# Kernel optimization log

Measured on AMD Instinct MI355X. Metric: run time of the kernel, lower is better.

The kernel has to match this reference:

```python
import jax, jax.numpy as jnp
import numpy as np

B, N = 4, 8192
D = 128
DEPTH = 4
LEAF = 32
HEADS = 4
HD = D // HEADS
SLOTS = 24
RANKS = [20, 32, 52, 82]                      # rank at encoder step j (fine -> coarse)
EXP = [RANKS[j] * (2 ** j) for j in range(DEPTH)]  # HODLR head output dims


def _rope_tables(seq_len, dim):
    inv_freq = 1.0 / (10000.0 ** (jnp.arange(0, dim, 2, dtype=jnp.float32) / dim))
    t = jnp.arange(seq_len, dtype=jnp.float32)
    freqs = t[:, None] * inv_freq[None, :]
    emb = jnp.concatenate([freqs, freqs], axis=-1)   # [S, dim]
    return jnp.cos(emb), jnp.sin(emb)


def _rotate_half(x):
    x1, x2 = jnp.split(x, 2, axis=-1)
    return jnp.concatenate([-x2, x1], axis=-1)


def _layernorm(x, g, b, eps=1e-5):
    mu = jnp.mean(x, -1, keepdims=True)
    var = jnp.mean((x - mu) ** 2, -1, keepdims=True)
    return (x - mu) * jax.lax.rsqrt(var + eps) * g + b


def _block_attn(h, qkv_w, qkv_b, pw, pb, cos, sin):
    Bc, Nc, C = h.shape
    nb = Nc // LEAF
    xb = h.reshape(Bc * nb, LEAF, C)
    qkv = (xb @ qkv_w + qkv_b).reshape(Bc * nb, LEAF, 3, HEADS, HD)
    qkv = qkv.transpose(2, 0, 3, 1, 4)               # [3, BN, H, L, hd]
    q, k, v = qkv[0], qkv[1], qkv[2]
    q = q * cos + _rotate_half(q) * sin              # full-dim RoPE (rope_dim == head_dim)
    k = k * cos + _rotate_half(k) * sin
    attn = jax.nn.softmax(jnp.einsum('bhqd,bhkd->bhqk', q, k) * (HD ** -0.5), axis=-1)
    o = jnp.einsum('bhqk,bhkd->bhqd', attn, v).transpose(0, 2, 1, 3).reshape(Bc * nb, LEAF, C)
    return (o @ pw + pb).reshape(Bc, Nc, C)


def _forward(x, cen_w, cen_b, nbr_w, nbr_b, inp_w, inp_b,
             leafp_w, leafp_b, leafh_w, leafh_b, log_scale_leaf,
             ln1_g, ln1_b, qkv_w, qkv_b, attnp_w, attnp_b,
             ln2_g, ln2_b, mlp1_w, mlp1_b, mlp2_w, mlp2_b, ds_w, ds_b,
             hu_w0, hu_b0, hv_w0, hv_b0, hu_w1, hu_b1, hv_w1, hv_b1,
             hu_w2, hu_b2, hv_w2, hv_b2, hu_w3, hu_b3, hv_w3, hv_b3):
    Bx, Nx, _ = x.shape
    # --- SymmetricNeighborEmbed (24 neighbor slots, vectorized) ---
    pos_i = x[..., 0:3]
    diag_i = x[..., 3:4]
    h_center = jnp.concatenate([pos_i, diag_i], -1) @ cen_w + cen_b          # [B,N,D]
    nb_feat = x[..., 4:4 + 5 * SLOTS].reshape(Bx, Nx, SLOTS, 5)
    rel = nb_feat[..., 0:1]
    pos_j = nb_feat[..., 1:4]
    w_ij = nb_feat[..., 4:5]
    active = (w_ij != 0.0).astype(x.dtype)
    feat = jnp.concatenate([rel * active, (pos_j - pos_i[:, :, None, :]) * active, w_ij], -1)
    e = (feat @ nbr_w + nbr_b) * active                                       # [B,N,24,D]
    h = h_center + jnp.sum(e, axis=2)
    h = h @ inp_w + inp_b
    # --- leaf dense diagonal blocks ---
    nl = Nx // LEAF
    hl = h.reshape(Bx, nl, LEAF, D) @ leafp_w + leafp_b                       # [B,nl,32,32]
    u_leaf = hl @ leafh_w + leafh_b
    dense = jnp.einsum('blik,bljk->blij', u_leaf, u_leaf) * jnp.exp(log_scale_leaf)
    diag_a = x[..., 3]                                                        # scale_A defaults to 1.0
    mask = jnp.abs(diag_a) > 1e-6
    new_diag = jnp.where(mask, 1.0 / jnp.where(mask, diag_a, 1.0), 1.0).reshape(Bx, nl, LEAF)
    dense = dense + new_diag[..., :, None] * jnp.eye(LEAF, dtype=x.dtype)
    # --- down-only encoder: transformer block -> HODLR head -> 2:1 downsample ---
    cos, sin = _rope_tables(LEAF, HD)
    hu = [(hu_w0, hu_b0), (hu_w1, hu_b1), (hu_w2, hu_b2), (hu_w3, hu_b3)]
    hv = [(hv_w0, hv_b0), (hv_w1, hv_b1), (hv_w2, hv_b2), (hv_w3, hv_b3)]
    us, vs = [], []
    for j in range(DEPTH):
        a = _block_attn(_layernorm(h, ln1_g[j], ln1_b[j]),
                        qkv_w[j], qkv_b[j], attnp_w[j], attnp_b[j], cos, sin)
        h = h + a
        m = _layernorm(h, ln2_g[j], ln2_b[j])
        m = jax.nn.gelu(m @ mlp1_w[j] + mlp1_b[j], approximate=False) @ mlp2_w[j] + mlp2_b[j]
        h = h + m
        us.append((h @ hu[j][0] + hu[j][1]).reshape(Bx, Nx, RANKS[j]))
        vs.append((h @ hv[j][0] + hv[j][1]).reshape(Bx, Nx, RANKS[j]))
        Bh, n, c = h.shape
        h = h.reshape(Bh, n // 2, 2 * c) @ ds_w[j] + ds_b[j]
    # single flat output: dense leaf blocks + all U/V HODLR factors
    return jnp.concatenate([dense.reshape(Bx, -1),
                            jnp.concatenate(us, -1).reshape(Bx, -1),
                            jnp.concatenate(vs, -1).reshape(Bx, -1)], -1)


def setup_inputs():
    key = jax.random.key(0)
    ks = iter(jax.random.split(key, 64))
    def rn(shape, s=0.05):
        return jax.random.normal(next(ks), shape, jnp.float32) * s
    z = lambda *s: jnp.zeros(s, jnp.float32)
    o = lambda *s: jnp.ones(s, jnp.float32)
    inp = {
        'x': jax.random.normal(next(ks), (B, N, 4 + 5 * SLOTS), jnp.float32),
        'cen_w': rn((4, D)), 'cen_b': z(D),
        'nbr_w': rn((5, D)), 'nbr_b': z(D),
        'inp_w': rn((D, D)), 'inp_b': z(D),
        'leafp_w': rn((D, LEAF)), 'leafp_b': z(LEAF),
        'leafh_w': rn((LEAF, LEAF), 0.01), 'leafh_b': z(LEAF),
        'log_scale_leaf': jnp.full((1,), np.log(0.01), jnp.float32),
        'ln1_g': o(DEPTH, D), 'ln1_b': z(DEPTH, D),
        'qkv_w': rn((DEPTH, D, 3 * D)), 'qkv_b': z(DEPTH, 3 * D),
        'attnp_w': rn((DEPTH, D, D)), 'attnp_b': z(DEPTH, D),
        'ln2_g': o(DEPTH, D), 'ln2_b': z(DEPTH, D),
        'mlp1_w': rn((DEPTH, D, 4 * D)), 'mlp1_b': z(DEPTH, 4 * D),
        'mlp2_w': rn((DEPTH, 4 * D, D)), 'mlp2_b': z(DEPTH, D),
        'ds_w': rn((DEPTH, 2 * D, D)), 'ds_b': z(DEPTH, D),
    }
    for j in range(DEPTH):
        inp['hu_w%d' % j] = rn((D, EXP[j]), 0.01)
        inp['hu_b%d' % j] = z(EXP[j])
        inp['hv_w%d' % j] = rn((D, EXP[j]), 0.01)
        inp['hv_b%d' % j] = z(EXP[j])
    return inp


def reference(x, cen_w, cen_b, nbr_w, nbr_b, inp_w, inp_b,
              leafp_w, leafp_b, leafh_w, leafh_b, log_scale_leaf,
              ln1_g, ln1_b, qkv_w, qkv_b, attnp_w, attnp_b,
              ln2_g, ln2_b, mlp1_w, mlp1_b, mlp2_w, mlp2_b, ds_w, ds_b,
              hu_w0, hu_b0, hv_w0, hv_b0, hu_w1, hu_b1, hv_w1, hv_b1,
              hu_w2, hu_b2, hv_w2, hv_b2, hu_w3, hu_b3, hv_w3, hv_b3):
    return _forward(x, cen_w, cen_b, nbr_w, nbr_b, inp_w, inp_b,
                    leafp_w, leafp_b, leafh_w, leafh_b, log_scale_leaf,
                    ln1_g, ln1_b, qkv_w, qkv_b, attnp_w, attnp_b,
                    ln2_g, ln2_b, mlp1_w, mlp1_b, mlp2_w, mlp2_b, ds_w, ds_b,
                    hu_w0, hu_b0, hv_w0, hv_b0, hu_w1, hu_b1, hv_w1, hv_b1,
                    hu_w2, hu_b2, hv_w2, hv_b2, hu_w3, hu_b3, hv_w3, hv_b3)
```

## Files before the change

kernel.cpp:

```cpp
#include <hip/hip_runtime.h>
#include <math.h>

#define DEV __device__ __forceinline__

constexpr int XFv = 124;
constexpr size_t OPB   = 3309568;
constexpr size_t UBASE = 262144;
constexpr size_t VBASE = 1785856;
constexpr int UVWID = 186;

using bfrag  = __attribute__((ext_vector_type(8))) short;
using f32x4v = __attribute__((ext_vector_type(4))) float;

DEV float* at4p(float* base, int t, int c0, int W) {
  return base + t * W + ((c0 + 4 * t) & (W - 1));
}
DEV float& at1r(float* base, int t, int c, int W) {
  return base[t * W + (((c & ~3) + 4 * t) & (W - 1)) + (c & 3)];
}
DEV float4 ld4g(const float* p) { return *(const float4*)p; }
DEV void fma4(float4& a, float s, const float4& w) {
  a.x += s * w.x; a.y += s * w.y; a.z += s * w.z; a.w += s * w.w;
}
DEV float gelu_fast(float x) {
  float x2 = x * x;
  float z = x * (1.5957691216057308f + 0.0713551f * x2);
  float e = __expf(z);
  float r = 1.0f - __frcp_rn(e + 1.0f);
  return x * r;
}
DEV ushort f2bf(float x) {
  unsigned u = __float_as_uint(x);
  unsigned r = (u + 0x7fffu + ((u >> 16) & 1u)) >> 16;
  return (ushort)r;
}
DEV void stb128(ushort* b, int row, int col, float v) {
  b[row * 128 + (((col & ~7) + 8 * row) & 127) + (col & 7)] = f2bf(v);
}

__global__ __launch_bounds__(256) void wprep_all_kernel(
    const float* __restrict__ src0, ushort* __restrict__ dst0, int K, int N) {
  size_t off = (size_t)blockIdx.z * K * N;
  const float* src = src0 + off;
  ushort* dst = dst0 + off;
  __shared__ float S[64][65];
  int tid = threadIdx.x;
  int k0 = blockIdx.x * 64, n0 = blockIdx.y * 64;
  for (int i = tid; i < 64 * 64; i += 256) {
    int kk = i >> 6, nn = i & 63;
    S[kk][nn] = src[(size_t)(k0 + kk) * N + n0 + nn];
  }
  __syncthreads();
  int n = tid >> 2, kq = tid & 3;
  unsigned pk[8];
#pragma unroll
  for (int i = 0; i < 8; i++) {
    int k = kq * 16 + 2 * i;
    pk[i] = (unsigned)f2bf(S[k][n]) | ((unsigned)f2bf(S[k + 1][n]) << 16);
  }
  unsigned* dp = (unsigned*)&dst[(size_t)(n0 + n) * K + k0 + kq * 16];
#pragma unroll
  for (int i = 0; i < 8; i++) dp[i] = pk[i];
}

struct UVDesc {
  const float* src[8];
  ushort* dst[8];
  int expj[8];
  int npad[8];
};
__global__ __launch_bounds__(256) void uvprep_all_kernel(UVDesc d) {
  int mi = blockIdx.y;
  int i = blockIdx.x * 256 + threadIdx.x;
  int expj = d.expj[mi];
  if (i >= d.npad[mi] * 128) return;
  int n = i >> 7, k = i & 127;
  d.dst[mi][(size_t)n * 128 + k] =
      (n < expj) ? f2bf(d.src[mi][(size_t)k * expj + n]) : (ushort)0;
}

__global__ __launch_bounds__(128) void weff_prep_kernel(
    const float* __restrict__ cw, const float* __restrict__ cb,
    const float* __restrict__ nw, const float* __restrict__ nb,
    const float* __restrict__ iw, const float* __restrict__ ib,
    float* __restrict__ weff, float* __restrict__ ropetab) {
  __shared__ float S[11 * 128];
  int tid = threadIdx.x;
  for (int i = tid; i < 512; i += 128) S[i] = cw[i];
  for (int i = tid; i < 640; i += 128) S[512 + i] = nw[i];
  S[1152 + tid] = nb[tid];
  S[1280 + tid] = cb[tid];
  __syncthreads();
  float acc[11];
#pragma unroll
  for (int r = 0; r < 10; r++) acc[r] = 0.f;
  acc[10] = ib[tid];
  for (int k = 0; k < 128; k++) {
    float w = iw[k * 128 + tid];
#pragma unroll
    for (int r = 0; r < 11; r++) acc[r] += S[r * 128 + k] * w;
  }
#pragma unroll
  for (int r = 0; r < 11; r++) weff[r * 128 + tid] = acc[r];
  for (int idx = tid; idx < 512; idx += 128) {
    int pos = idx >> 4, d = idx & 15;
    float ang = (float)pos * expf(-0.57564627324851148f * (float)d);
    ropetab[idx] = cosf(ang);
    ropetab[512 + idx] = sinf(ang);
  }
}

__global__ __launch_bounds__(256) void node_embed2_kernel(
    const float* __restrict__ x, const float* __restrict__ weff,
    float* __restrict__ h) {
  __shared__ float XR[64 * XFv];
  __shared__ float RF[64][11];
  __shared__ __align__(16) float WE[11 * 128];
  int tid = threadIdx.x;
  int node0 = blockIdx.x * 64;
  for (int i = tid; i < 64 * XFv; i += 256)
    XR[i] = x[(size_t)node0 * XFv + i];
  for (int i = tid; i < 11 * 128; i += 256) WE[i] = weff[i];
  __syncthreads();
  {
    int nn = tid >> 2, sl = tid & 3;
    const float* xr = XR + nn * XFv;
    float p0 = xr[0], p1 = xr[1], p2 = xr[2];
    float g[6] = {0.f, 0.f, 0.f, 0.f, 0.f, 0.f};
#pragma unroll
    for (int s = 0; s < 6; s++) {
      const float* f = xr + 4 + 5 * (sl * 6 + s);
      float w = f[4];
      if (w != 0.0f) {
        g[0] += f[0]; g[1] += f[1] - p0; g[2] += f[2] - p1;
        g[3] += f[3] - p2; g[4] += w; g[5] += 1.0f;
      }
    }
#pragma unroll
    for (int i = 0; i < 6; i++) {
      g[i] += __shfl_xor(g[i], 1);
      g[i] += __shfl_xor(g[i], 2);
    }
    if (sl == 0) {
      RF[nn][0] = p0; RF[nn][1] = p1; RF[nn][2] = p2; RF[nn][3] = xr[3];
#pragma unroll
      for (int i = 0; i < 6; i++) RF[nn][4 + i] = g[i];
    }
  }
  __syncthreads();
  {
    int w = tid >> 6, lane = tid & 63;
    int c4 = lane & 31, hi = lane >> 5;
    const float4* WE4 = (const float4*)WE;
#pragma unroll
    for (int rr = 0; rr < 8; rr++) {
      int node = w * 16 + rr * 2 + hi;
      float4 acc = WE4[10 * 32 + c4];
#pragma unroll
      for (int f = 0; f < 10; f++)
        fma4(acc, RF[node][f], WE4[f * 32 + c4]);
      *(float4*)&h[(size_t)(node0 + node) * 128 + c4 * 4] = acc;
    }
  }
}

__global__ __launch_bounds__(256) void leaf_dense_kernel(
    const float* __restrict__ h, const float* __restrict__ x,
    const float* __restrict__ lpw, const float* __restrict__ lpb,
    const float* __restrict__ lhw, const float* __restrict__ lhb,
    const float* __restrict__ lsc, float* __restrict__ out) {
  __shared__ __align__(16) float HS[32 * 128];
  __shared__ __align__(16) float HL[32 * 32];
  __shared__ __align__(16) float UL[32 * 32];
  int tid = threadIdx.x;
  int leaf = blockIdx.x;
  size_t base = (size_t)leaf * (32 * 128);
  for (int i = tid; i < 32 * 128; i += 256) {
    int t = i >> 7, c = i & 127;
    at1r(HS, t, c, 128) = h[base + i];
  }
  __syncthreads();
  int t = tid & 31, cg = tid >> 5;
  {
    float4 acc = ld4g(&lpb[4 * cg]);
    for (int k4 = 0; k4 < 128; k4 += 4) {
      float4 xv = *(const float4*)at4p(HS, t, k4, 128);
      float xa[4] = {xv.x, xv.y, xv.z, xv.w};
#pragma unroll
      for (int kk = 0; kk < 4; kk++)
        fma4(acc, xa[kk], ld4g(&lpw[(k4 + kk) * 32 + 4 * cg]));
    }
    *(float4*)at4p(HL, t, 4 * cg, 32) = acc;
  }
  __syncthreads();
  {
    float4 acc = ld4g(&lhb[4 * cg]);
    for (int k4 = 0; k4 < 32; k4 += 4) {
      float4 xv = *(const float4*)at4p(HL, t, k4, 32);
      float xa[4] = {xv.x, xv.y, xv.z, xv.w};
#pragma unroll
      for (int kk = 0; kk < 4; kk++)
        fma4(acc, xa[kk], ld4g(&lhw[(k4 + kk) * 32 + 4 * cg]));
    }
    *(float4*)at4p(UL, t, 4 * cg, 32) = acc;
  }
  __syncthreads();
  {
    float scale = expf(lsc[0]);
    float acc[4] = {0.f, 0.f, 0.f, 0.f};
    for (int k4 = 0; k4 < 32; k4 += 4) {
      float4 xv = *(const float4*)at4p(UL, t, k4, 32);
      float xa[4] = {xv.x, xv.y, xv.z, xv.w};
#pragma unroll
      for (int kk = 0; kk < 4; kk++) {
        int k = k4 + kk;
#pragma unroll
        for (int i2 = 0; i2 < 4; i2++)
          acc[i2] += xa[kk] * at1r(UL, 4 * cg + i2, k, 32);
      }
    }
    int b = leaf >> 8, l = leaf & 255;
#pragma unroll
    for (int i2 = 0; i2 < 4; i2++) {
      int c = 4 * cg + i2;
      float v = acc[i2] * scale;
      if (c == t) {
        float dg = x[(size_t)(leaf * 32 + t) * XFv + 3];
        v += (fabsf(dg) > 1e-6f) ? (1.0f / dg) : 1.0f;
      }
      out[(size_t)b * OPB + (size_t)l * 1024 + t * 32 + c] = v;
    }
  }
}

__global__ __launch_bounds__(256) void attn_mfma_kernel(
    float* __restrict__ h,
    const float* __restrict__ lng, const float* __restrict__ lnb,
    const ushort* __restrict__ wqkvt, const float* __restrict__ bqkv,
    const ushort* __restrict__ wpt, const float* __restrict__ pb,
    const float* __restrict__ rt) {
  __shared__ __align__(16) ushort XN[64 * 128];
  __shared__ __align__(16) ushort QB[64 * 128];
  __shared__ __align__(16) ushort KB[64 * 128];
  __shared__ __align__(16) ushort VT[128 * 64];
  int tid = threadIdx.x;
  size_t base = (size_t)blockIdx.x * (64 * 128);

  {
    int m = tid >> 2, p = tid & 3;
    const float* row = h + base + m * 128 + p * 32;
    float v[32];
    float s = 0.f;
#pragma unroll
    for (int i = 0; i < 32; i += 4) {
      float4 t4 = ld4g(row + i);
      v[i] = t4.x; v[i + 1] = t4.y; v[i + 2] = t4.z; v[i + 3] = t4.w;
      s += t4.x + t4.y + t4.z + t4.w;
    }
    s += __shfl_xor(s, 1); s += __shfl_xor(s, 2);
    float mu = s * (1.0f / 128.0f);
    float s2 = 0.f;
#pragma unroll
    for (int i = 0; i < 32; i++) { float d = v[i] - mu; s2 += d * d; }
    s2 += __shfl_xor(s2, 1); s2 += __shfl_xor(s2, 2);
    float rs = rsqrtf(s2 * (1.0f / 128.0f) + 1e-5f);
    unsigned* XW = (unsigned*)XN;
#pragma unroll
    for (int i = 0; i < 32; i += 2) {
      int c = p * 32 + i;
      float x0 = (v[i] - mu) * rs * lng[c] + lnb[c];
      float x1 = (v[i + 1] - mu) * rs * lng[c + 1] + lnb[c + 1];
      int kp = c >> 1;
      XW[m * 64 + ((kp + 4 * m) & 63)] =
          (unsigned)f2bf(x0) | ((unsigned)f2bf(x1) << 16);
    }
  }
  __syncthreads();

  int w = tid >> 6, l = tid & 63, lm = l & 15, q = l >> 4;

  {
    f32x4v acc[4][6];
#pragma unroll
    for (int mt = 0; mt < 4; mt++)
#pragma unroll
      for (int nt = 0; nt < 6; nt++) acc[mt][nt] = (f32x4v){0.f, 0.f, 0.f, 0.f};
    for (int ks = 0; ks < 4; ks++) {
      bfrag a[4];
#pragma unroll
      for (int mt = 0; mt < 4; mt++) {
        int mm = mt * 16 + lm;
        a[mt] = *(const bfrag*)&XN[mm * 128 + ((ks * 32 + q * 8 + 8 * mm) & 127)];
      }
#pragma unroll
      for (int nt = 0; nt < 6; nt++) {
        int n = w * 96 + nt * 16 + lm;
        bfrag b = *(const bfrag*)&wqkvt[(size_t)n * 128 + ks * 32 + q * 8];
#pragma unroll
        for (int mt = 0; mt < 4; mt++)
          acc[mt][nt] = __builtin_amdgcn_mfma_f32_16x16x32_bf16(
              a[mt], b, acc[mt][nt], 0, 0, 0);
      }
    }
    float csA[4] = {}, snA[4] = {}, csB[4] = {}, snB[4] = {};
    if (w < 3) {
#pragma unroll
      for (int r = 0; r < 4; r++) {
        int pa = q * 4 + r;
        csA[r] = rt[pa * 16 + lm];        snA[r] = rt[512 + pa * 16 + lm];
        csB[r] = rt[(pa + 16) * 16 + lm]; snB[r] = rt[512 + (pa + 16) * 16 + lm];
      }
    }
#pragma unroll
    for (int p2 = 0; p2 < 3; p2++) {
      int g = w * 6 + 2 * p2;
      int ne = g * 16 + lm;
      if (g < 16) {
        float be = bqkv[ne], bo = bqkv[ne + 16];
        ushort* dst = (g < 8) ? QB : KB;
        int de = (g < 8) ? ne : ne - 128;
#pragma unroll
        for (int mt = 0; mt < 4; mt++)
#pragma unroll
          for (int r = 0; r < 4; r++) {
            int mm = mt * 16 + q * 4 + r;
            float cs = (mt & 1) ? csB[r] : csA[r];
            float sn = (mt & 1) ? snB[r] : snA[r];
            float e = acc[mt][2 * p2][r] + be;
            float o = acc[mt][2 * p2 + 1][r] + bo;
            stb128(dst, mm, de, e * cs - o * sn);
            stb128(dst, mm, de + 16, o * cs + e * sn);
          }
      } else {
#pragma unroll
        for (int h2 = 0; h2 < 2; h2++) {
          int nt = 2 * p2 + h2;
          int nv = (g + h2) * 16 + lm;
          int dv = nv - 256;
          float bv = bqkv[nv];
#pragma unroll
          for (int mt = 0; mt < 4; mt++) {
            int t0 = mt * 16 + q * 4;
            short4 pk;
            pk.x = (short)f2bf(acc[mt][nt][0] + bv);
            pk.y = (short)f2bf(acc[mt][nt][1] + bv);
            pk.z = (short)f2bf(acc[mt][nt][2] + bv);
            pk.w = (short)f2bf(acc[mt][nt][3] + bv);
            *(short4*)&VT[dv * 64 + (((t0 & ~7) + 8 * dv) & 63) + (t0 & 7)] = pk;
          }
        }
      }
    }
  }
  __syncthreads();

  ushort* SP = XN;
  {
#pragma unroll
    for (int ci = 0; ci < 2; ci++) {
      int combo = w + 4 * ci;
      int head = combo >> 1, leaf = combo & 1;
      f32x4v sc[2][2];
#pragma unroll
      for (int a2 = 0; a2 < 2; a2++)
#pragma unroll
        for (int b2 = 0; b2 < 2; b2++) sc[a2][b2] = (f32x4v){0.f, 0.f, 0.f, 0.f};
      bfrag qa[2], kb[2];
#pragma unroll
      for (int mt2 = 0; mt2 < 2; mt2++) {
        int row = leaf * 32 + mt2 * 16 + lm;
        qa[mt2] = *(const bfrag*)&QB[row * 128 + ((head * 32 + q * 8 + 8 * row) & 127)];
      }
#pragma unroll
      for (int nt2 = 0; nt2 < 2; nt2++) {
        int kt = leaf * 32 + nt2 * 16 + lm;
        kb[nt2] = *(const bfrag*)&KB[kt * 128 + ((head * 32 + q * 8 + 8 * kt) & 127)];
      }
#pragma unroll
      for (int mt2 = 0; mt2 < 2; mt2++)
#pragma unroll
        for (int nt2 = 0; nt2 < 2; nt2++)
          sc[mt2][nt2] = __builtin_amdgcn_mfma_f32_16x16x32_bf16(
              qa[mt2], kb[nt2], sc[mt2][nt2], 0, 0, 0);
      const float scl = 0.17677669529663688f;
#pragma unroll
      for (int mt2 = 0; mt2 < 2; mt2++)
#pragma unroll
        for (int nt2 = 0; nt2 < 2; nt2++)
#pragma unroll
          for (int r = 0; r < 4; r++) {
            int qt = leaf * 32 + mt2 * 16 + q * 4 + r;
            int kc = nt2 * 16 + lm;
            SP[head * 2048 + qt * 32 + (((kc & ~7) + 8 * qt) & 31) + (kc & 7)] =
                f2bf(sc[mt2][nt2][r] * scl);
          }
    }
  }
  __syncthreads();

  {
    int head = tid >> 6, qt = tid & 63;
    ushort* rowp = SP + head * 2048 + qt * 32;
    float v[32];
#pragma unroll
    for (int pc = 0; pc < 4; pc++) {
      uint4 ch = *(const uint4*)&rowp[pc * 8];
      unsigned uu[4] = {ch.x, ch.y, ch.z, ch.w};
#pragma unroll
      for (int i2 = 0; i2 < 4; i2++) {
        v[pc * 8 + 2 * i2]     = __uint_as_float(uu[i2] << 16);
        v[pc * 8 + 2 * i2 + 1] = __uint_as_float(uu[i2] & 0xffff0000u);
      }
    }
    float mx = -1e30f;
#pragma unroll
    for (int i = 0; i < 32; i++) mx = fmaxf(mx, v[i]);
    float s = 0.f;
#pragma unroll
    for (int i = 0; i < 32; i++) { v[i] = __expf(v[i] - mx); s += v[i]; }
    float inv = 1.0f / s;
#pragma unroll
    for (int pc = 0; pc < 4; pc++) {
      uint4 ch;
      unsigned uu[4];
#pragma unroll
      for (int i2 = 0; i2 < 4; i2++)
        uu[i2] = (unsigned)f2bf(v[pc * 8 + 2 * i2] * inv) |
                 ((unsigned)f2bf(v[pc * 8 + 2 * i2 + 1] * inv) << 16);
      ch.x = uu[0]; ch.y = uu[1]; ch.z = uu[2]; ch.w = uu[3];
      *(uint4*)&rowp[pc * 8] = ch;
    }
  }
  __syncthreads();

  ushort* OB = QB;
  {
#pragma unroll
    for (int ci = 0; ci < 2; ci++) {
      int combo = w + 4 * ci;
      int head = combo >> 1, leaf = combo & 1;
      f32x4v ov[2][2];
#pragma unroll
      for (int a2 = 0; a2 < 2; a2++)
#pragma unroll
        for (int b2 = 0; b2 < 2; b2++) ov[a2][b2] = (f32x4v){0.f, 0.f, 0.f, 0.f};
      bfrag pa[2], vb[2];
#pragma unroll
      for (int mt2 = 0; mt2 < 2; mt2++) {
        int qt = leaf * 32 + mt2 * 16 + lm;
        pa[mt2] = *(const bfrag*)&SP[head * 2048 + qt * 32 + ((q * 8 + 8 * qt) & 31)];
      }
#pragma unroll
      for (int nt2 = 0; nt2 < 2; nt2++) {
        int gdim = head * 32 + nt2 * 16 + lm;
        int t0 = leaf * 32 + q * 8;
        vb[nt2] = *(const bfrag*)&VT[gdim * 64 + ((t0 + 8 * gdim) & 63)];
      }
#pragma unroll
      for (int mt2 = 0; mt2 < 2; mt2++)
#pragma unroll
        for (int nt2 = 0; nt2 < 2; nt2++)
          ov[mt2][nt2] = __builtin_amdgcn_mfma_f32_16x16x32_bf16(
              pa[mt2], vb[nt2], ov[mt2][nt2], 0, 0, 0);
#pragma unroll
      for (int mt2 = 0; mt2 < 2; mt2++)
#pragma unroll
        for (int nt2 = 0; nt2 < 2; nt2++)
#pragma unroll
          for (int r = 0; r < 4; r++) {
            int qt = leaf * 32 + mt2 * 16 + q * 4 + r;
            int gdim = head * 32 + nt2 * 16 + lm;
            stb128(OB, qt, gdim, ov[mt2][nt2][r]);
          }
    }
  }
  __syncthreads();

  {
    f32x4v po[4][2];
#pragma unroll
    for (int mt = 0; mt < 4; mt++)
#pragma unroll
      for (int nt = 0; nt < 2; nt++) po[mt][nt] = (f32x4v){0.f, 0.f, 0.f, 0.f};
    for (int ks = 0; ks < 4; ks++) {
      bfrag a[4];
#pragma unroll
      for (int mt = 0; mt < 4; mt++) {
        int mm = mt * 16 + lm;
        a[mt] = *(const bfrag*)&OB[mm * 128 + ((ks * 32 + q * 8 + 8 * mm) & 127)];
      }
#pragma unroll
      for (int nt = 0; nt < 2; nt++) {
        int n = w * 32 + nt * 16 + lm;
        bfrag b = *(const bfrag*)&wpt[(size_t)n * 128 + ks * 32 + q * 8];
#pragma unroll
        for (int mt = 0; mt < 4; mt++)
          po[mt][nt] = __builtin_amdgcn_mfma_f32_16x16x32_bf16(
              a[mt], b, po[mt][nt], 0, 0, 0);
      }
    }
#pragma unroll
    for (int nt = 0; nt < 2; nt++) {
      int n = w * 32 + nt * 16 + lm;
      float bv = pb[n];
#pragma unroll
      for (int mt = 0; mt < 4; mt++)
#pragma unroll
        for (int r = 0; r < 4; r++) {
          int mm = mt * 16 + q * 4 + r;
          float* gp = h + base + (size_t)mm * 128 + n;
          *gp = *gp + po[mt][nt][r] + bv;
        }
    }
  }
}

__global__ __launch_bounds__(256) void mlp_mfma_kernel(
    float* __restrict__ h,
    const float* __restrict__ lng, const float* __restrict__ lnb,
    const ushort* __restrict__ w1t, const float* __restrict__ b1,
    const ushort* __restrict__ w2t, const float* __restrict__ b2) {
  __shared__ __align__(16) ushort XN[64 * 128];
  __shared__ __align__(16) ushort HC[64 * 128];
  int tid = threadIdx.x;
  size_t base = (size_t)blockIdx.x * (64 * 128);

  {
    int m = tid >> 2, p = tid & 3;
    const float* row = h + base + m * 128 + p * 32;
    float v[32];
    float s = 0.f;
#pragma unroll
    for (int i = 0; i < 32; i += 4) {
      float4 t4 = ld4g(row + i);
      v[i] = t4.x; v[i + 1] = t4.y; v[i + 2] = t4.z; v[i + 3] = t4.w;
      s += t4.x + t4.y + t4.z + t4.w;
    }
    s += __shfl_xor(s, 1); s += __shfl_xor(s, 2);
    float mu = s * (1.0f / 128.0f);
    float s2 = 0.f;
#pragma unroll
    for (int i = 0; i < 32; i++) { float d = v[i] - mu; s2 += d * d; }
    s2 += __shfl_xor(s2, 1); s2 += __shfl_xor(s2, 2);
    float rs = rsqrtf(s2 * (1.0f / 128.0f) + 1e-5f);
    unsigned* XW = (unsigned*)XN;
#pragma unroll
    for (int i = 0; i < 32; i += 2) {
      int c = p * 32 + i;
      float x0 = (v[i] - mu) * rs * lng[c] + lnb[c];
      float x1 = (v[i + 1] - mu) * rs * lng[c + 1] + lnb[c + 1];
      int kp = c >> 1;
      XW[m * 64 + ((kp + 4 * m) & 63)] =
          (unsigned)f2bf(x0) | ((unsigned)f2bf(x1) << 16);
    }
  }
  __syncthreads();

  int w = tid >> 6, l = tid & 63, lm = l & 15, q = l >> 4;

  f32x4v acc2[4][2];
#pragma unroll
  for (int mt = 0; mt < 4; mt++)
#pragma unroll
    for (int nt = 0; nt < 2; nt++) acc2[mt][nt] = (f32x4v){0.f, 0.f, 0.f, 0.f};

  for (int hc = 0; hc < 4; hc++) {
    f32x4v acc1[4][2];
#pragma unroll
    for (int mt = 0; mt < 4; mt++)
#pragma unroll
      for (int nt = 0; nt < 2; nt++) acc1[mt][nt] = (f32x4v){0.f, 0.f, 0.f, 0.f};
#pragma unroll
    for (int ks = 0; ks < 4; ks++) {
      bfrag a[4];
#pragma unroll
      for (int mt = 0; mt < 4; mt++) {
        int mm = mt * 16 + lm;
        a[mt] = *(const bfrag*)&XN[mm * 128 + ((ks * 32 + q * 8 + 8 * mm) & 127)];
      }
#pragma unroll
      for (int nt = 0; nt < 2; nt++) {
        int n = hc * 128 + w * 32 + nt * 16 + lm;
        bfrag b = *(const bfrag*)&w1t[(size_t)n * 128 + ks * 32 + q * 8];
#pragma unroll
        for (int mt = 0; mt < 4; mt++)
          acc1[mt][nt] = __builtin_amdgcn_mfma_f32_16x16x32_bf16(
              a[mt], b, acc1[mt][nt], 0, 0, 0);
      }
    }
    if (hc) __syncthreads();
#pragma unroll
    for (int nt = 0; nt < 2; nt++) {
      int nl = w * 32 + nt * 16 + lm;
      float b1v = b1[hc * 128 + nl];
#pragma unroll
      for (int mt = 0; mt < 4; mt++)
#pragma unroll
        for (int r = 0; r < 4; r++) {
          int mm = mt * 16 + q * 4 + r;
          float val = gelu_fast(acc1[mt][nt][r] + b1v);
          HC[mm * 128 + (((nl & ~7) + 8 * mm) & 127) + (nl & 7)] = f2bf(val);
        }
    }
    __syncthreads();
#pragma unroll
    for (int ks = 0; ks < 4; ks++) {
      bfrag a[4];
#pragma unroll
      for (int mt = 0; mt < 4; mt++) {
        int mm = mt * 16 + lm;
        a[mt] = *(const bfrag*)&HC[mm * 128 + ((ks * 32 + q * 8 + 8 * mm) & 127)];
      }
#pragma unroll
      for (int nt = 0; nt < 2; nt++) {
        int n = w * 32 + nt * 16 + lm;
        bfrag b = *(const bfrag*)&w2t[(size_t)n * 512 + hc * 128 + ks * 32 + q * 8];
#pragma unroll
        for (int mt = 0; mt < 4; mt++)
          acc2[mt][nt] = __builtin_amdgcn_mfma_f32_16x16x32_bf16(
              a[mt], b, acc2[mt][nt], 0, 0, 0);
      }
    }
  }

#pragma unroll
  for (int nt = 0; nt < 2; nt++) {
    int n = w * 32 + nt * 16 + lm;
    float b2v = b2[n];
#pragma unroll
    for (int mt = 0; mt < 4; mt++)
#pragma unroll
      for (int r = 0; r < 4; r++) {
        int mm = mt * 16 + q * 4 + r;
        float* gp = h + base + (size_t)mm * 128 + n;
        *gp = *gp + acc2[mt][nt][r] + b2v;
      }
  }
}

template <int EXPJ, int RANK, int LVL, int NSPLIT>
__global__ __launch_bounds__(256) void uv_mfma_kernel(
    const float* __restrict__ h,
    const ushort* __restrict__ uwt, const float* __restrict__ ub,
    const ushort* __restrict__ vwt, const float* __restrict__ vb,
    float* __restrict__ out, int Nj) {
  constexpr int NT16 = (EXPJ + 15) / 16;
  constexpr int NJOBS = 2 * NT16;
  constexpr int COFF = (LVL == 0) ? 0 : (LVL == 1) ? 20 : (LVL == 2) ? 52 : 104;
  __shared__ __align__(16) ushort XN[64 * 128];
  int tid = threadIdx.x;
  int t0 = blockIdx.x * 64;
  size_t base = (size_t)t0 * 128;
  {
    int m = tid >> 2, p = tid & 3;
    const float* row = h + base + m * 128 + p * 32;
    unsigned* XW = (unsigned*)XN;
#pragma unroll
    for (int i = 0; i < 32; i += 4) {
      float4 t4 = ld4g(row + i);
      int kp = (p * 32 + i) >> 1;
      XW[m * 64 + ((kp + 4 * m) & 63)] =
          (unsigned)f2bf(t4.x) | ((unsigned)f2bf(t4.y) << 16);
      XW[m * 64 + ((kp + 1 + 4 * m) & 63)] =
          (unsigned)f2bf(t4.z) | ((unsigned)f2bf(t4.w) << 16);
    }
  }
  __syncthreads();
  int bidx = t0 / Nj;
  int tl0 = t0 - bidx * Nj;
  size_t obase = (size_t)bidx * OPB;
  int w = tid >> 6, l = tid & 63, lm = l & 15, q = l >> 4;
  int gw = w + 4 * blockIdx.y;
  for (int jj = gw; jj < NJOBS; jj += 4 * NSPLIT) {
    int uvsel = jj & 1, nt = jj >> 1;
    const ushort* wt = uvsel ? vwt : uwt;
    const float* bias = uvsel ? vb : ub;
    size_t ob = obase + (uvsel ? VBASE : UBASE);
    f32x4v acc[4];
#pragma unroll
    for (int mt = 0; mt < 4; mt++) acc[mt] = (f32x4v){0.f, 0.f, 0.f, 0.f};
    for (int ks = 0; ks < 4; ks++) {
      bfrag b = *(const bfrag*)&wt[(size_t)(nt * 16 + lm) * 128 + ks * 32 + q * 8];
#pragma unroll
      for (int mt = 0; mt < 4; mt++) {
        int mm = mt * 16 + lm;
        int ke = ks * 32 + q * 8;
        bfrag a = *(const bfrag*)&XN[mm * 128 + ((ke + 8 * mm) & 127)];
        acc[mt] = __builtin_amdgcn_mfma_f32_16x16x32_bf16(a, b, acc[mt], 0, 0, 0);
      }
    }
    int c = nt * 16 + lm;
    if (c < EXPJ) {
      float bv = bias[c];
      int cdiv = c / RANK, cmod = c - cdiv * RANK;
#pragma unroll
      for (int mt = 0; mt < 4; mt++)
#pragma unroll
        for (int r = 0; r < 4; r++) {
          int mm = mt * 16 + q * 4 + r;
          int nrow = ((tl0 + mm) << LVL) + cdiv;
          out[ob + (size_t)nrow * UVWID + COFF + cmod] = acc[mt][r] + bv;
        }
    }
  }
}

__global__ __launch_bounds__(256) void ds_mfma_kernel(
    const float* __restrict__ hin, float* __restrict__ hout,
    const ushort* __restrict__ wt, const float* __restrict__ bias) {
  __shared__ __align__(16) ushort XN[64 * 256];
  int tid = threadIdx.x;
  size_t base = (size_t)blockIdx.x * (64 * 256);
  {
    int m = tid >> 2, p = tid & 3;
    const float* row = hin + base + m * 256 + p * 64;
    unsigned* XW = (unsigned*)XN;
#pragma unroll
    for (int i = 0; i < 64; i += 4) {
      float4 t4 = ld4g(row + i);
      int kp = (p * 64 + i) >> 1;
      XW[m * 128 + ((kp + 4 * m) & 127)] =
          (unsigned)f2bf(t4.x) | ((unsigned)f2bf(t4.y) << 16);
      XW[m * 128 + ((kp + 1 + 4 * m) & 127)] =
          (unsigned)f2bf(t4.z) | ((unsigned)f2bf(t4.w) << 16);
    }
  }
  __syncthreads();
  int w = tid >> 6, l = tid & 63, lm = l & 15, q = l >> 4;
  f32x4v acc[4][2];
#pragma unroll
  for (int mt = 0; mt < 4; mt++)
#pragma unroll
    for (int nt = 0; nt < 2; nt++) acc[mt][nt] = (f32x4v){0.f, 0.f, 0.f, 0.f};
  for (int ks = 0; ks < 8; ks++) {
    bfrag a[4];
#pragma unroll
    for (int mt = 0; mt < 4; mt++) {
      int mm = mt * 16 + lm;
      a[mt] = *(const bfrag*)&XN[mm * 256 + ((ks * 32 + q * 8 + 8 * mm) & 255)];
    }
#pragma unroll
    for (int nt = 0; nt < 2; nt++) {
      int n = w * 32 + nt * 16 + lm;
      bfrag b = *(const bfrag*)&wt[(size_t)n * 256 + ks * 32 + q * 8];
#pragma unroll
      for (int mt = 0; mt < 4; mt++)
        acc[mt][nt] = __builtin_amdgcn_mfma_f32_16x16x32_bf16(
            a[mt], b, acc[mt][nt], 0, 0, 0);
    }
  }
  size_t obase = (size_t)blockIdx.x * (64 * 128);
#pragma unroll
  for (int nt = 0; nt < 2; nt++) {
    int n = w * 32 + nt * 16 + lm;
    float bv = bias[n];
#pragma unroll
    for (int mt = 0; mt < 4; mt++)
#pragma unroll
      for (int r = 0; r < 4; r++) {
        int mm = mt * 16 + q * 4 + r;
        hout[obase + (size_t)mm * 128 + n] = acc[mt][nt][r] + bv;
      }
  }
}

extern "C" void kernel_launch(void* const* d_in, const int* in_sizes, int n_in,
                              void* d_out, int out_size, void* d_ws, size_t ws_size,
                              hipStream_t stream) {
  const float* x       = (const float*)d_in[0];
  const float* cen_w   = (const float*)d_in[1];
  const float* cen_b   = (const float*)d_in[2];
  const float* nbr_w   = (const float*)d_in[3];
  const float* nbr_b   = (const float*)d_in[4];
  const float* inp_w   = (const float*)d_in[5];
  const float* inp_b   = (const float*)d_in[6];
  const float* leafp_w = (const float*)d_in[7];
  const float* leafp_b = (const float*)d_in[8];
  const float* leafh_w = (const float*)d_in[9];
  const float* leafh_b = (const float*)d_in[10];
  const float* lscale  = (const float*)d_in[11];
  const float* ln1_g   = (const float*)d_in[12];
  const float* ln1_b   = (const float*)d_in[13];
  const float* qkv_w   = (const float*)d_in[14];
  const float* qkv_b   = (const float*)d_in[15];
  const float* attnp_w = (const float*)d_in[16];
  const float* attnp_b = (const float*)d_in[17];
  const float* ln2_g   = (const float*)d_in[18];
  const float* ln2_b   = (const float*)d_in[19];
  const float* mlp1_w  = (const float*)d_in[20];
  const float* mlp1_b  = (const float*)d_in[21];
  const float* mlp2_w  = (const float*)d_in[22];
  const float* mlp2_b  = (const float*)d_in[23];
  const float* ds_w    = (const float*)d_in[24];
  const float* ds_b    = (const float*)d_in[25];
  const float* huw[4], *hub[4], *hvw[4], *hvb[4];
  for (int j = 0; j < 4; j++) {
    huw[j] = (const float*)d_in[26 + 4 * j];
    hub[j] = (const float*)d_in[27 + 4 * j];
    hvw[j] = (const float*)d_in[28 + 4 * j];
    hvb[j] = (const float*)d_in[29 + 4 * j];
  }
  float* out = (float*)d_out;
  float* hA = (float*)d_ws;
  float* hB = hA + (size_t)4 * 8192 * 128;
  ushort* w1t = (ushort*)(hB + (size_t)2097152);
  ushort* w2t = w1t + (size_t)4 * 65536;
  ushort* uvt = w2t + (size_t)4 * 65536;
  const int NPAD[4] = {32, 64, 208, 656};
  ushort* uwt[4]; ushort* vwt[4];
  ushort* p = uvt;
  for (int j = 0; j < 4; j++) {
    uwt[j] = p; p += (size_t)NPAD[j] * 128;
    vwt[j] = p; p += (size_t)NPAD[j] * 128;
  }
  ushort* wqkvt = p;
  ushort* wpt   = wqkvt + (size_t)4 * 384 * 128;
  ushort* dswt  = wpt + (size_t)4 * 128 * 128;
  float* weff   = (float*)(dswt + (size_t)4 * 128 * 256);
  float* ropetab = weff + 1408;
  const int EXPJ_[4] = {20, 64, 208, 656};

  weff_prep_kernel<<<1, 128, 0, stream>>>(
      cen_w, cen_b, nbr_w, nbr_b, inp_w, inp_b, weff, ropetab);
  wprep_all_kernel<<<dim3(2, 8, 4), 256, 0, stream>>>(mlp1_w, w1t, 128, 512);
  wprep_all_kernel<<<dim3(8, 2, 4), 256, 0, stream>>>(mlp2_w, w2t, 512, 128);
  wprep_all_kernel<<<dim3(2, 6, 4), 256, 0, stream>>>(qkv_w, wqkvt, 128, 384);
  wprep_all_kernel<<<dim3(2, 2, 4), 256, 0, stream>>>(attnp_w, wpt, 128, 128);
  wprep_all_kernel<<<dim3(4, 2, 4), 256, 0, stream>>>(ds_w, dswt, 256, 128);
  {
    UVDesc d;
    for (int j = 0; j < 4; j++) {
      d.src[2 * j] = huw[j];     d.dst[2 * j] = uwt[j];
      d.src[2 * j + 1] = hvw[j]; d.dst[2 * j + 1] = vwt[j];
      d.expj[2 * j] = EXPJ_[j];  d.expj[2 * j + 1] = EXPJ_[j];
      d.npad[2 * j] = NPAD[j];   d.npad[2 * j + 1] = NPAD[j];
    }
    uvprep_all_kernel<<<dim3(328, 8), 256, 0, stream>>>(d);
  }

  node_embed2_kernel<<<(4 * 8192) / 64, 256, 0, stream>>>(x, weff, hA);
  leaf_dense_kernel<<<(4 * 8192) / 32, 256, 0, stream>>>(
      hA, x, leafp_w, leafp_b, leafh_w, leafh_b, lscale, out);

  float* cur = hA;
  float* nxt = hB;
  int Nj = 8192;
  for (int j = 0; j < 4; j++) {
    int tokens = 4 * Nj;
    attn_mfma_kernel<<<tokens / 64, 256, 0, stream>>>(
        cur, ln1_g + j * 128, ln1_b + j * 128,
        wqkvt + (size_t)j * 49152, qkv_b + j * 384,
        wpt + (size_t)j * 16384, attnp_b + j * 128, ropetab);
    mlp_mfma_kernel<<<tokens / 64, 256, 0, stream>>>(
        cur, ln2_g + j * 128, ln2_b + j * 128,
        w1t + (size_t)j * 65536, mlp1_b + j * 512,
        w2t + (size_t)j * 65536, mlp2_b + j * 128);
    if (j == 0)
      uv_mfma_kernel<20, 20, 0, 1><<<dim3(tokens / 64, 1), 256, 0, stream>>>(
          cur, uwt[0], hub[0], vwt[0], hvb[0], out, Nj);
    else if (j == 1)
      uv_mfma_kernel<64, 32, 1, 2><<<dim3(tokens / 64, 2), 256, 0, stream>>>(
          cur, uwt[1], hub[1], vwt[1], hvb[1], out, Nj);
    else if (j == 2)
      uv_mfma_kernel<208, 52, 2, 4><<<dim3(tokens / 64, 4), 256, 0, stream>>>(
          cur, uwt[2], hub[2], vwt[2], hvb[2], out, Nj);
    else
      uv_mfma_kernel<656, 82, 3, 8><<<dim3(tokens / 64, 8), 256, 0, stream>>>(
          cur, uwt[3], hub[3], vwt[3], hvb[3], out, Nj);
    ds_mfma_kernel<<<tokens / 128, 256, 0, stream>>>(
        cur, nxt, dswt + (size_t)j * 32768, ds_b + j * 128);
    float* tmp = cur; cur = nxt; nxt = tmp;
    Nj >>= 1;
  }
  (void)in_sizes; (void)n_in; (void)out_size; (void)ws_size;
}
```

Before: 484.3 us.

## Fuse attention and MLP sublayers into one per-tile transformer layer kernel

Merges the attention kernel and the MLP kernel into a single kernel per 64-token tile. The attention output plus residual is kept in shared memory (aliased over the K/V buffers), LayerNorm2 is computed from that, and only the final residual sum is written back to global memory. This removes one launch per depth level and a global read-modify-write round trip of the hidden state. In exchange the kernel uses a larger 64KB shared buffer, which may reduce occupancy, and has higher register pressure.

```diff
diff --git a/kernel.cpp b/kernel.cpp
--- a/kernel.cpp
+++ b/kernel.cpp
@@ -233,16 +233,21 @@
   }
 }
 
-__global__ __launch_bounds__(256) void attn_mfma_kernel(
+__global__ __launch_bounds__(256) void layer_mfma_kernel(
     float* __restrict__ h,
     const float* __restrict__ lng, const float* __restrict__ lnb,
     const ushort* __restrict__ wqkvt, const float* __restrict__ bqkv,
     const ushort* __restrict__ wpt, const float* __restrict__ pb,
-    const float* __restrict__ rt) {
-  __shared__ __align__(16) ushort XN[64 * 128];
-  __shared__ __align__(16) ushort QB[64 * 128];
-  __shared__ __align__(16) ushort KB[64 * 128];
-  __shared__ __align__(16) ushort VT[128 * 64];
+    const float* __restrict__ rt,
+    const float* __restrict__ ln2g, const float* __restrict__ ln2b,
+    const ushort* __restrict__ w1t, const float* __restrict__ b1,
+    const ushort* __restrict__ w2t, const float* __restrict__ b2) {
+  __shared__ __align__(16) ushort SM[32768];
+  ushort* XN = SM;
+  ushort* QB = SM + 8192;
+  ushort* KB = SM + 16384;
+  ushort* VT = SM + 24576;
+  float*  HS = (float*)(SM + 16384);
   int tid = threadIdx.x;
   size_t base = (size_t)blockIdx.x * (64 * 128);
 
@@ -508,56 +513,51 @@
 #pragma unroll
         for (int r = 0; r < 4; r++) {
           int mm = mt * 16 + q * 4 + r;
-          float* gp = h + base + (size_t)mm * 128 + n;
-          *gp = *gp + po[mt][nt][r] + bv;
+          HS[mm * 128 + n] = po[mt][nt][r] + bv;
         }
     }
   }
-}
-
-__global__ __launch_bounds__(256) void mlp_mfma_kernel(
-    float* __restrict__ h,
-    const float* __restrict__ lng, const float* __restrict__ lnb,
-    const ushort* __restrict__ w1t, const float* __restrict__ b1,
-    const ushort* __restrict__ w2t, const float* __restrict__ b2) {
-  __shared__ __align__(16) ushort XN[64 * 128];
-  __shared__ __align__(16) ushort HC[64 * 128];
-  int tid = threadIdx.x;
-  size_t base = (size_t)blockIdx.x * (64 * 128);
-
-  {
-    int m = tid >> 2, p = tid & 3;
-    const float* row = h + base + m * 128 + p * 32;
-    float v[32];
-    float s = 0.f;
-#pragma unroll
-    for (int i = 0; i < 32; i += 4) {
-      float4 t4 = ld4g(row + i);
-      v[i] = t4.x; v[i + 1] = t4.y; v[i + 2] = t4.z; v[i + 3] = t4.w;
-      s += t4.x + t4.y + t4.z + t4.w;
-    }
-    s += __shfl_xor(s, 1); s += __shfl_xor(s, 2);
-    float mu = s * (1.0f / 128.0f);
-    float s2 = 0.f;
-#pragma unroll
-    for (int i = 0; i < 32; i++) { float d = v[i] - mu; s2 += d * d; }
-    s2 += __shfl_xor(s2, 1); s2 += __shfl_xor(s2, 2);
-    float rs = rsqrtf(s2 * (1.0f / 128.0f) + 1e-5f);
+  __syncthreads();
+
+  {
+    int j = tid & 31;
+    int c0 = j * 4;
+    float g0 = ln2g[c0], g1 = ln2g[c0 + 1], g2 = ln2g[c0 + 2], g3 = ln2g[c0 + 3];
+    float e0 = ln2b[c0], e1 = ln2b[c0 + 1], e2 = ln2b[c0 + 2], e3 = ln2b[c0 + 3];
     unsigned* XW = (unsigned*)XN;
 #pragma unroll
-    for (int i = 0; i < 32; i += 2) {
-      int c = p * 32 + i;
-      float x0 = (v[i] - mu) * rs * lng[c] + lnb[c];
-      float x1 = (v[i + 1] - mu) * rs * lng[c + 1] + lnb[c + 1];
-      int kp = c >> 1;
-      XW[m * 64 + ((kp + 4 * m) & 63)] =
+    for (int k2 = 0; k2 < 8; k2++) {
+      int idx = tid + 256 * k2;
+      int tok = idx >> 5;
+      float4 hg = ld4g(&h[base + (size_t)idx * 4]);
+      float4 ao = *(const float4*)&HS[idx * 4];
+      float4 hn;
+      hn.x = hg.x + ao.x; hn.y = hg.y + ao.y;
+      hn.z = hg.z + ao.z; hn.w = hg.w + ao.w;
+      *(float4*)&HS[idx * 4] = hn;
+      float s = hn.x + hn.y + hn.z + hn.w;
+      s += __shfl_xor(s, 1); s += __shfl_xor(s, 2); s += __shfl_xor(s, 4);
+      s += __shfl_xor(s, 8); s += __shfl_xor(s, 16);
+      float mu = s * (1.0f / 128.0f);
+      float d0 = hn.x - mu, d1 = hn.y - mu, d2 = hn.z - mu, d3 = hn.w - mu;
+      float s2 = d0 * d0 + d1 * d1 + d2 * d2 + d3 * d3;
+      s2 += __shfl_xor(s2, 1); s2 += __shfl_xor(s2, 2); s2 += __shfl_xor(s2, 4);
+      s2 += __shfl_xor(s2, 8); s2 += __shfl_xor(s2, 16);
+      float rs = rsqrtf(s2 * (1.0f / 128.0f) + 1e-5f);
+      float x0 = d0 * rs * g0 + e0;
+      float x1 = d1 * rs * g1 + e1;
+      float x2 = d2 * rs * g2 + e2;
+      float x3 = d3 * rs * g3 + e3;
+      int kp = 2 * j;
+      XW[tok * 64 + ((kp + 4 * tok) & 63)] =
           (unsigned)f2bf(x0) | ((unsigned)f2bf(x1) << 16);
-    }
-  }
-  __syncthreads();
-
-  int w = tid >> 6, l = tid & 63, lm = l & 15, q = l >> 4;
-
+      XW[tok * 64 + ((kp + 1 + 4 * tok) & 63)] =
+          (unsigned)f2bf(x2) | ((unsigned)f2bf(x3) << 16);
+    }
+  }
+  __syncthreads();
+
+  ushort* HC = QB;
   f32x4v acc2[4][2];
 #pragma unroll
   for (int mt = 0; mt < 4; mt++)
@@ -632,8 +632,7 @@
 #pragma unroll
       for (int r = 0; r < 4; r++) {
         int mm = mt * 16 + q * 4 + r;
-        float* gp = h + base + (size_t)mm * 128 + n;
-        *gp = *gp + acc2[mt][nt][r] + b2v;
+        h[base + (size_t)mm * 128 + n] = HS[mm * 128 + n] + acc2[mt][nt][r] + b2v;
       }
   }
 }
@@ -847,12 +846,11 @@
   int Nj = 8192;
   for (int j = 0; j < 4; j++) {
     int tokens = 4 * Nj;
-    attn_mfma_kernel<<<tokens / 64, 256, 0, stream>>>(
+    layer_mfma_kernel<<<tokens / 64, 256, 0, stream>>>(
         cur, ln1_g + j * 128, ln1_b + j * 128,
         wqkvt + (size_t)j * 49152, qkv_b + j * 384,
-        wpt + (size_t)j * 16384, attnp_b + j * 128, ropetab);
-    mlp_mfma_kernel<<<tokens / 64, 256, 0, stream>>>(
-        cur, ln2_g + j * 128, ln2_b + j * 128,
+        wpt + (size_t)j * 16384, attnp_b + j * 128, ropetab,
+        ln2_g + j * 128, ln2_b + j * 128,
         w1t + (size_t)j * 65536, mlp1_b + j * 512,
         w2t + (size_t)j * 65536, mlp2_b + j * 128);
     if (j == 0)
```

Result: faster. 470.4 us (-2.9%).
